# Optimization experiments

Hardware: AMD Instinct MI355X
Metric: run time of the kernel (lower is better)

Reference implementation:

```python
import jax, jax.numpy as jnp
import numpy as np


def setup_inputs() -> dict:
    key = jax.random.key(0)
    k1, k2 = jax.random.split(key)
    B, C, H, W = 32, 8, 256, 256
    inp = jax.random.normal(k1, (B, C, H, W), dtype=jnp.float32)
    tgt = jax.random.uniform(k2, (B, C, H, W), dtype=jnp.float32)
    return {"input": inp, "target": tgt}


def reference(input, target):
    B, C, H, W = input.shape
    # DSNT: softmax over each flattened heatmap -> expected (x, y) coords
    probs = jax.nn.softmax(input.reshape(B, C, H * W), axis=-1).reshape(B, C, H, W)
    xs = (jnp.arange(1, W + 1, dtype=input.dtype) / W)  # (j+1)/x_size
    ys = (jnp.arange(1, H + 1, dtype=input.dtype) / H)  # (p+1)/y_size
    pred_x = jnp.einsum('bchw,w->bc', probs, xs)
    pred_y = jnp.einsum('bchw,h->bc', probs, ys)
    # ground truth: argmax of target heatmap -> grid coords
    am = jnp.argmax(target.reshape(B, C, H * W), axis=-1)  # [B,C] int
    true_x = ((am % W) + 1).astype(input.dtype) / W
    true_y = ((am // W) + 1).astype(input.dtype) / H
    ed = jnp.sqrt((true_x - pred_x) ** 2 + (true_y - pred_y) ** 2)  # [B,C]
    # original sums over all (b,c) and divides by (i+1) == batch size B
    return (jnp.sum(ed) / B).reshape(1)
```

## Files before the change

kernel.cpp:

```cpp
#include <hip/hip_runtime.h>
#include <float.h>
#include <math.h>


#define HW 65536
#define BLOCK 1024
#define F4_PER_THREAD 16

__global__ __launch_bounds__(BLOCK) void dsnt_loss_kernel(
    const float* __restrict__ inp,
    const float* __restrict__ tgt,
    float* __restrict__ out)
{
    const int bc = blockIdx.x;
    const int t  = threadIdx.x;
    const float4* in4 = (const float4*)(inp + (size_t)bc * HW);
    const float4* tg4 = (const float4*)(tgt + (size_t)bc * HW);

    const float inv256 = 1.0f / 256.0f;

    float m = -FLT_MAX, l = 0.0f, sx = 0.0f, sy = 0.0f;
    float bv = -FLT_MAX;
    int   bi = 0;

#pragma unroll
    for (int k = 0; k < F4_PER_THREAD; ++k) {
        const int f4 = t + k * BLOCK;
        const float4 x = in4[f4];
        const float4 g = tg4[f4];
        const int e0 = f4 * 4;

        const float m4 = fmaxf(fmaxf(x.x, x.y), fmaxf(x.z, x.w));
        const float mn = fmaxf(m, m4);
        const float c  = __expf(m - mn);
        const float ex = __expf(x.x - mn);
        const float ey = __expf(x.y - mn);
        const float ez = __expf(x.z - mn);
        const float ew = __expf(x.w - mn);
        const float es = (ex + ey) + (ez + ew);

        const int   w0 = e0 & 255;
        const int   hh = e0 >> 8;
        const float ysw = (float)(hh + 1) * inv256;
        const float sxl = ex * (float)(w0 + 1) + ey * (float)(w0 + 2)
                        + ez * (float)(w0 + 3) + ew * (float)(w0 + 4);

        l  = l  * c + es;
        sy = sy * c + ysw * es;
        sx = sx * c + sxl * inv256;
        m  = mn;

        if (g.x > bv) { bv = g.x; bi = e0;     }
        if (g.y > bv) { bv = g.y; bi = e0 + 1; }
        if (g.z > bv) { bv = g.z; bi = e0 + 2; }
        if (g.w > bv) { bv = g.w; bi = e0 + 3; }
    }

#pragma unroll
    for (int off = 32; off > 0; off >>= 1) {
        const float m2  = __shfl_down(m,  off);
        const float l2  = __shfl_down(l,  off);
        const float sx2 = __shfl_down(sx, off);
        const float sy2 = __shfl_down(sy, off);
        const float bv2 = __shfl_down(bv, off);
        const int   bi2 = __shfl_down(bi, off);

        const float mn = fmaxf(m, m2);
        const float c1 = __expf(m  - mn);
        const float c2 = __expf(m2 - mn);
        l  = l  * c1 + l2  * c2;
        sx = sx * c1 + sx2 * c2;
        sy = sy * c1 + sy2 * c2;
        m  = mn;
        if (bv2 > bv || (bv2 == bv && bi2 < bi)) { bv = bv2; bi = bi2; }
    }

    __shared__ float sm[16], sl[16], ssx[16], ssy[16], sbv[16];
    __shared__ int   sbi[16];
    const int wid  = t >> 6;
    const int lane = t & 63;
    if (lane == 0) {
        sm[wid] = m; sl[wid] = l; ssx[wid] = sx; ssy[wid] = sy;
        sbv[wid] = bv; sbi[wid] = bi;
    }
    __syncthreads();

    if (t == 0) {
        m = sm[0]; l = sl[0]; sx = ssx[0]; sy = ssy[0]; bv = sbv[0]; bi = sbi[0];
#pragma unroll
        for (int i = 1; i < 16; ++i) {
            const float mi = sm[i];
            const float mn = fmaxf(m, mi);
            const float c1 = __expf(m  - mn);
            const float c2 = __expf(mi - mn);
            l  = l  * c1 + sl[i]  * c2;
            sx = sx * c1 + ssx[i] * c2;
            sy = sy * c1 + ssy[i] * c2;
            m  = mn;
            if (sbv[i] > bv || (sbv[i] == bv && sbi[i] < bi)) { bv = sbv[i]; bi = sbi[i]; }
        }
        const float px = sx / l;
        const float py = sy / l;
        const float tx = (float)((bi & 255) + 1) * inv256;
        const float ty = (float)((bi >> 8) + 1) * inv256;
        const float dx = tx - px;
        const float dy = ty - py;
        const float ed = sqrtf(dx * dx + dy * dy);
        atomicAdd(out, ed * (1.0f / 32.0f));
    }
}

extern "C" void kernel_launch(void* const* d_in, const int* in_sizes, int n_in,
                              void* d_out, int out_size, void* d_ws, size_t ws_size,
                              hipStream_t stream) {
    const float* inp = (const float*)d_in[0];
    const float* tgt = (const float*)d_in[1];
    float* out = (float*)d_out;

    const int n_heatmaps = in_sizes[0] / HW;

    hipMemsetAsync(out, 0, sizeof(float), stream);
    dsnt_loss_kernel<<<n_heatmaps, BLOCK, 0, stream>>>(inp, tgt, out);
}
```

Before: 148.4 us.

## Split each heatmap across four blocks and combine partials in a final kernel

Each heatmap is now processed by four 512-thread blocks instead of one 1024-thread block, giving 1024 blocks so more work is in flight across the 256 CUs. Per-chunk online-softmax and argmax partials go to the workspace, and a second single-block kernel merges them and reduces the loss without atomics or a memset. The cost is an extra kernel launch and a small workspace round trip. The final kernel handles at most 256 heatmaps.

```diff
diff --git a/kernel.cpp b/kernel.cpp
--- a/kernel.cpp
+++ b/kernel.cpp
@@ -4,18 +4,25 @@
 
 
 #define HW 65536
-#define BLOCK 1024
-#define F4_PER_THREAD 16
+#define SPLITS 4
+#define K1_BLOCK 512
+#define CHUNK (HW / SPLITS)
+#define F4_PER_THREAD (CHUNK / 4 / K1_BLOCK)
 
-__global__ __launch_bounds__(BLOCK) void dsnt_loss_kernel(
+__global__ __launch_bounds__(K1_BLOCK) void dsnt_partial_kernel(
     const float* __restrict__ inp,
     const float* __restrict__ tgt,
-    float* __restrict__ out)
+    float* __restrict__ ws,
+    int np)
 {
-    const int bc = blockIdx.x;
-    const int t  = threadIdx.x;
-    const float4* in4 = (const float4*)(inp + (size_t)bc * HW);
-    const float4* tg4 = (const float4*)(tgt + (size_t)bc * HW);
+    const int blk = blockIdx.x;
+    const int bc  = blk >> 2;
+    const int s   = blk & 3;
+    const int t   = threadIdx.x;
+
+    const float4* in4 = (const float4*)(inp + (size_t)bc * HW) + s * (CHUNK / 4);
+    const float4* tg4 = (const float4*)(tgt + (size_t)bc * HW) + s * (CHUNK / 4);
+    const int ebase = s * CHUNK;
 
     const float inv256 = 1.0f / 256.0f;
 
@@ -25,10 +32,10 @@
 
 #pragma unroll
     for (int k = 0; k < F4_PER_THREAD; ++k) {
-        const int f4 = t + k * BLOCK;
+        const int f4 = t + k * K1_BLOCK;
         const float4 x = in4[f4];
         const float4 g = tg4[f4];
-        const int e0 = f4 * 4;
+        const int e0 = ebase + f4 * 4;
 
         const float m4 = fmaxf(fmaxf(x.x, x.y), fmaxf(x.z, x.w));
         const float mn = fmaxf(m, m4);
@@ -75,8 +82,8 @@
         if (bv2 > bv || (bv2 == bv && bi2 < bi)) { bv = bv2; bi = bi2; }
     }
 
-    __shared__ float sm[16], sl[16], ssx[16], ssy[16], sbv[16];
-    __shared__ int   sbi[16];
+    __shared__ float sm[8], sl[8], ssx[8], ssy[8], sbv[8];
+    __shared__ int   sbi[8];
     const int wid  = t >> 6;
     const int lane = t & 63;
     if (lane == 0) {
@@ -88,7 +95,7 @@
     if (t == 0) {
         m = sm[0]; l = sl[0]; sx = ssx[0]; sy = ssy[0]; bv = sbv[0]; bi = sbi[0];
 #pragma unroll
-        for (int i = 1; i < 16; ++i) {
+        for (int i = 1; i < 8; ++i) {
             const float mi = sm[i];
             const float mn = fmaxf(m, mi);
             const float c1 = __expf(m  - mn);
@@ -99,15 +106,64 @@
             m  = mn;
             if (sbv[i] > bv || (sbv[i] == bv && sbi[i] < bi)) { bv = sbv[i]; bi = sbi[i]; }
         }
+        ws[blk]          = m;
+        ws[np + blk]     = l;
+        ws[2 * np + blk] = sx;
+        ws[3 * np + blk] = sy;
+        ws[4 * np + blk] = bv;
+        ((int*)ws)[5 * np + blk] = bi;
+    }
+}
+
+__global__ __launch_bounds__(256) void dsnt_final_kernel(
+    const float* __restrict__ ws,
+    float* __restrict__ out,
+    int nbc, int np)
+{
+    const int i = threadIdx.x;
+    const float inv256 = 1.0f / 256.0f;
+    float ed = 0.0f;
+
+    if (i < nbc) {
+        const int j0 = i * SPLITS;
+        float m  = ws[j0];
+        float l  = ws[np + j0];
+        float sx = ws[2 * np + j0];
+        float sy = ws[3 * np + j0];
+        float bv = ws[4 * np + j0];
+        int   bi = ((const int*)ws)[5 * np + j0];
+#pragma unroll
+        for (int j = 1; j < SPLITS; ++j) {
+            const int jj = j0 + j;
+            const float mj = ws[jj];
+            const float mn = fmaxf(m, mj);
+            const float c1 = __expf(m  - mn);
+            const float c2 = __expf(mj - mn);
+            l  = l  * c1 + ws[np + jj]     * c2;
+            sx = sx * c1 + ws[2 * np + jj] * c2;
+            sy = sy * c1 + ws[3 * np + jj] * c2;
+            m  = mn;
+            const float bvj = ws[4 * np + jj];
+            if (bvj > bv) { bv = bvj; bi = ((const int*)ws)[5 * np + jj]; }
+        }
         const float px = sx / l;
         const float py = sy / l;
         const float tx = (float)((bi & 255) + 1) * inv256;
         const float ty = (float)((bi >> 8) + 1) * inv256;
         const float dx = tx - px;
         const float dy = ty - py;
-        const float ed = sqrtf(dx * dx + dy * dy);
-        atomicAdd(out, ed * (1.0f / 32.0f));
+        ed = sqrtf(dx * dx + dy * dy);
     }
+
+#pragma unroll
+    for (int off = 32; off > 0; off >>= 1)
+        ed += __shfl_down(ed, off);
+
+    __shared__ float sw[4];
+    if ((i & 63) == 0) sw[i >> 6] = ed;
+    __syncthreads();
+    if (i == 0)
+        out[0] = (sw[0] + sw[1] + sw[2] + sw[3]) * (1.0f / 32.0f);
 }
 
 extern "C" void kernel_launch(void* const* d_in, const int* in_sizes, int n_in,
@@ -116,9 +172,11 @@
     const float* inp = (const float*)d_in[0];
     const float* tgt = (const float*)d_in[1];
     float* out = (float*)d_out;
+    float* ws  = (float*)d_ws;
 
-    const int n_heatmaps = in_sizes[0] / HW;
+    const int nbc = in_sizes[0] / HW;
+    const int np  = nbc * SPLITS;
 
-    hipMemsetAsync(out, 0, sizeof(float), stream);
-    dsnt_loss_kernel<<<n_heatmaps, BLOCK, 0, stream>>>(inp, tgt, out);
+    dsnt_partial_kernel<<<np, K1_BLOCK, 0, stream>>>(inp, tgt, ws, np);
+    dsnt_final_kernel<<<1, 256, 0, stream>>>(ws, out, nbc, np);
 }
```

Measured after the change: 148.4 us. No clear change (+0.0%).
